# Optimization experiments

Measured on AMD Instinct MI355X. Metric: run time of the kernel, lower is better.

Reference implementation:

```python
import jax, jax.numpy as jnp
import numpy as np

N_NODES = 50000
N_EDGES = 800000
IN_CH = 512
HIDDEN = 512


def setup_inputs() -> dict:
    key = jax.random.key(0)
    k1, k2, k3, k4 = jax.random.split(key, 4)
    x = jax.random.normal(k1, (N_NODES, IN_CH), dtype=jnp.float32)
    edge_index = jax.random.randint(k2, (2, N_EDGES), 0, N_NODES, dtype=jnp.int64)
    # Glorot-style scaling for weights
    W1 = jax.random.normal(k3, (IN_CH, HIDDEN), dtype=jnp.float32) / np.sqrt(IN_CH)
    b1 = jnp.zeros((HIDDEN,), dtype=jnp.float32)
    W2 = jax.random.normal(k4, (HIDDEN, 1), dtype=jnp.float32) / np.sqrt(HIDDEN)
    b2 = jnp.zeros((1,), dtype=jnp.float32)
    return {"x": x, "edge_index": edge_index, "W1": W1, "b1": b1, "W2": W2, "b2": b2}


def _gcn_conv(x, edge_index, W, b):
    """PyG GCNConv: add self-loops, symmetric D^{-1/2}(A+I)D^{-1/2} normalization."""
    N = x.shape[0]
    xw = x @ W                                   # [N, out]
    row, col = edge_index[0], edge_index[1]      # source -> target
    # degree on target nodes, +1 for the self-loop
    deg = jax.ops.segment_sum(jnp.ones_like(col, dtype=xw.dtype), col, num_segments=N) + 1.0
    dis = jax.lax.rsqrt(deg)                     # deg^{-1/2}, [N]
    norm = dis[row] * dis[col]                   # [E]
    agg = jax.ops.segment_sum(norm[:, None] * xw[row], col, num_segments=N)
    agg = agg + (dis * dis)[:, None] * xw        # self-loop contribution
    return agg + b


def reference(x, edge_index, W1, b1, W2, b2):
    h = jax.nn.relu(_gcn_conv(x, edge_index, W1, b1))
    # dropout in eval mode (training=False) -> identity
    out = _gcn_conv(h, edge_index, W2, b2)
    return out.squeeze(-1)                       # [N]
```

## Files before the change

kernel.cpp:

```cpp
#include <hip/hip_runtime.h>

#define IN_CH 512
#define SCAN_BLK 1024

typedef _Float16 f16x8 __attribute__((ext_vector_type(8)));
typedef float f32x4 __attribute__((ext_vector_type(4)));

__device__ __forceinline__ void gload_lds16(const void* g, void* l) {
    __builtin_amdgcn_global_load_lds(
        (const __attribute__((address_space(1))) unsigned int*)g,
        (__attribute__((address_space(3))) unsigned int*)l, 16, 0, 0);
}

__global__ void k_deg(const int* __restrict__ col, int* __restrict__ deg,
                      int E, int N) {
    int e = blockIdx.x * blockDim.x + threadIdx.x;
    if (e < E) {
        int d = col[e];
        if ((unsigned)d < (unsigned)N) atomicAdd(&deg[d], 1);
    }
}

__global__ __launch_bounds__(SCAN_BLK) void k_psum(const int* __restrict__ deg,
                                                   int* __restrict__ bsum, int N) {
    __shared__ int red[SCAN_BLK / 64];
    int i = blockIdx.x * SCAN_BLK + threadIdx.x;
    int v = (i < N) ? deg[i] : 0;
#pragma unroll
    for (int off = 32; off > 0; off >>= 1) v += __shfl_down(v, off);
    if ((threadIdx.x & 63) == 0) red[threadIdx.x >> 6] = v;
    __syncthreads();
    if (threadIdx.x == 0) {
        int s = 0;
#pragma unroll
        for (int u = 0; u < SCAN_BLK / 64; ++u) s += red[u];
        bsum[blockIdx.x] = s;
    }
}

__global__ __launch_bounds__(SCAN_BLK) void k_write(const int* __restrict__ deg,
                                                    const int* __restrict__ bsum,
                                                    int* __restrict__ rp,
                                                    float* __restrict__ dis,
                                                    int* __restrict__ cursor, int N) {
    __shared__ int sums[SCAN_BLK];
    __shared__ int boff_s, tot_s;
    int t = threadIdx.x;
    if (t < 64) {
        int v = (t < (int)gridDim.x) ? bsum[t] : 0;
        int pre = (t < (int)blockIdx.x) ? v : 0;
        int a = pre, b = v;
#pragma unroll
        for (int off = 32; off > 0; off >>= 1) {
            a += __shfl_down(a, off);
            b += __shfl_down(b, off);
        }
        if (t == 0) { boff_s = a; tot_s = b; }
    }
    int i = blockIdx.x * SCAN_BLK + t;
    int d = (i < N) ? deg[i] : 0;
    sums[t] = d;
    __syncthreads();
    for (int off = 1; off < SCAN_BLK; off <<= 1) {
        int u = (t >= off) ? sums[t - off] : 0;
        __syncthreads();
        sums[t] += u;
        __syncthreads();
    }
    if (i < N) {
        rp[i] = boff_s + sums[t] - d;
        dis[i] = rsqrtf((float)d + 1.0f);
        cursor[i] = 0;
    }
    if (blockIdx.x == gridDim.x - 1 && t == 0) rp[N] = tot_s;
}

__global__ void k_fill(const int* __restrict__ ei, const int* __restrict__ rp,
                       int* __restrict__ cursor, int* __restrict__ csrc,
                       int E, int N) {
    int e = blockIdx.x * blockDim.x + threadIdx.x;
    if (e < E) {
        int s = ei[e];
        int d = ei[E + e];
        if ((unsigned)s < (unsigned)N && (unsigned)d < (unsigned)N) {
            int pos = atomicAdd(&cursor[d], 1);
            csrc[rp[d] + pos] = s;
        }
    }
}

__global__ __launch_bounds__(256) void k_cvt_w(const float* __restrict__ W1,
                                               _Float16* __restrict__ W1t) {
    __shared__ float tile[32][33];
    const int bk = blockIdx.x * 32, bn = blockIdx.y * 32;
    const int tx = threadIdx.x & 31, ty = threadIdx.x >> 5;
#pragma unroll
    for (int p = 0; p < 4; ++p)
        tile[ty + p * 8][tx] = W1[(size_t)(bk + ty + p * 8) * 512 + bn + tx];
    __syncthreads();
#pragma unroll
    for (int p = 0; p < 4; ++p)
        W1t[(size_t)(bn + ty + p * 8) * 512 + bk + tx] = (_Float16)tile[tx][ty + p * 8];
}

__global__ __launch_bounds__(256) void k_gemm(const float* __restrict__ A,
                                              const _Float16* __restrict__ Bt,
                                              const float* __restrict__ dis,
                                              _Float16* __restrict__ C,
                                              int Nrows, int nbm) {
    __shared__ __align__(16) _Float16 As[128 * 64];
    __shared__ __align__(16) _Float16 Bs[128 * 64];
    const int t = threadIdx.x;
    const int lane = t & 63, w = t >> 6;
    const int wm = w >> 1, wn = w & 1;

    const int nwg = nbm * 4;
    const int q = nwg >> 3, r = nwg & 7;
    const int xcd = blockIdx.x & 7, within = blockIdx.x >> 3;
    const int wg = (xcd < r ? xcd * (q + 1) : r * (q + 1) + (xcd - r) * q) + within;
    const int bm = (wg >> 2) * 128, bn = (wg & 3) * 128;

    const int rr = lane & 15, kg = lane >> 4;
    const int lrow = lane >> 3, lcol = (lane & 7) * 8;
    const int arow = t >> 3, acol = (t & 7) * 8;

    f32x4 acc[4][4];
#pragma unroll
    for (int i = 0; i < 4; ++i)
#pragma unroll
        for (int j = 0; j < 4; ++j) acc[i][j] = (f32x4)0.0f;

    for (int k0 = 0; k0 < 512; k0 += 64) {
#pragma unroll
        for (int p = 0; p < 4; ++p) {
            const int row = p * 32 + w * 8 + lrow;
            gload_lds16(Bt + (size_t)(bn + row) * 512 + k0 + lcol,
                        Bs + (p * 32 + w * 8) * 64);
        }
#pragma unroll
        for (int p = 0; p < 4; ++p) {
            int grow = bm + p * 32 + arow;
            if (grow >= Nrows) grow = Nrows - 1;
            const float* gp = A + (size_t)grow * 512 + k0 + acol;
            float4 u0 = *(const float4*)gp;
            float4 u1 = *(const float4*)(gp + 4);
            f16x8 o;
            o[0] = (_Float16)u0.x; o[1] = (_Float16)u0.y;
            o[2] = (_Float16)u0.z; o[3] = (_Float16)u0.w;
            o[4] = (_Float16)u1.x; o[5] = (_Float16)u1.y;
            o[6] = (_Float16)u1.z; o[7] = (_Float16)u1.w;
            *(f16x8*)(As + ((p * 32 + arow) * 64 + acol)) = o;
        }
        __syncthreads();
#pragma unroll
        for (int kk = 0; kk < 2; ++kk) {
            f16x8 a[4], b[4];
#pragma unroll
            for (int i = 0; i < 4; ++i)
                a[i] = *(const f16x8*)(As + (wm * 64 + i * 16 + rr) * 64 + kk * 32 + kg * 8);
#pragma unroll
            for (int j = 0; j < 4; ++j)
                b[j] = *(const f16x8*)(Bs + (wn * 64 + j * 16 + rr) * 64 + kk * 32 + kg * 8);
#pragma unroll
            for (int i = 0; i < 4; ++i)
#pragma unroll
                for (int j = 0; j < 4; ++j)
                    acc[i][j] = __builtin_amdgcn_mfma_f32_16x16x32_f16(a[i], b[j], acc[i][j], 0, 0, 0);
        }
        __syncthreads();
    }

#pragma unroll
    for (int i = 0; i < 4; ++i)
#pragma unroll
        for (int reg = 0; reg < 4; ++reg) {
            int m = bm + wm * 64 + i * 16 + kg * 4 + reg;
            int mc = (m < Nrows) ? m : Nrows - 1;
            float dm = dis[mc];
#pragma unroll
            for (int j = 0; j < 4; ++j) {
                int n = bn + wn * 64 + j * 16 + rr;
                C[(size_t)m * 512 + n] = (_Float16)(acc[i][j][reg] * dm);
            }
        }
}

__global__ __launch_bounds__(256) void k_agg(const _Float16* __restrict__ y,
                                             const float* __restrict__ dis,
                                             const int* __restrict__ rp,
                                             const int* __restrict__ csrc,
                                             const float* __restrict__ b1,
                                             const float* __restrict__ W2,
                                             float* __restrict__ z, int N) {
    const int n = blockIdx.x * 4 + (threadIdx.x >> 6);
    if (n >= N) return;
    const int l = threadIdx.x & 63;

    const float d1 = dis[n];
    f16x8 self = *(const f16x8*)(y + (size_t)n * 512 + l * 8);
    float acc[8];
#pragma unroll
    for (int c = 0; c < 8; ++c) acc[c] = (float)self[c];

    int j = rp[n], jend = rp[n + 1];
    for (; j + 8 <= jend; j += 8) {
        int s[8]; f16x8 v[8];
#pragma unroll
        for (int u = 0; u < 8; ++u) s[u] = csrc[j + u];
#pragma unroll
        for (int u = 0; u < 8; ++u)
            v[u] = *(const f16x8*)(y + (size_t)s[u] * 512 + l * 8);
#pragma unroll
        for (int u = 0; u < 8; ++u)
#pragma unroll
            for (int c = 0; c < 8; ++c) acc[c] += (float)v[u][c];
    }
    for (; j + 2 <= jend; j += 2) {
        int s0 = csrc[j], s1 = csrc[j + 1];
        f16x8 v0 = *(const f16x8*)(y + (size_t)s0 * 512 + l * 8);
        f16x8 v1 = *(const f16x8*)(y + (size_t)s1 * 512 + l * 8);
#pragma unroll
        for (int c = 0; c < 8; ++c) acc[c] += (float)v0[c] + (float)v1[c];
    }
    if (j < jend) {
        f16x8 v0 = *(const f16x8*)(y + (size_t)csrc[j] * 512 + l * 8);
#pragma unroll
        for (int c = 0; c < 8; ++c) acc[c] += (float)v0[c];
    }

    float4 bb0 = *(const float4*)(b1 + l * 8);
    float4 bb1 = *(const float4*)(b1 + l * 8 + 4);
    float4 w20 = *(const float4*)(W2 + l * 8);
    float4 w21 = *(const float4*)(W2 + l * 8 + 4);
    float bbv[8] = {bb0.x, bb0.y, bb0.z, bb0.w, bb1.x, bb1.y, bb1.z, bb1.w};
    float w2v[8] = {w20.x, w20.y, w20.z, w20.w, w21.x, w21.y, w21.z, w21.w};
    float p = 0.0f;
#pragma unroll
    for (int c = 0; c < 8; ++c) {
        float h = fmaxf(acc[c] * d1 + bbv[c], 0.0f);
        p += h * w2v[c];
    }
#pragma unroll
    for (int off = 32; off > 0; off >>= 1) p += __shfl_down(p, off);
    if (l == 0) z[n] = d1 * p;
}

__global__ void k_out(const float* __restrict__ z, const float* __restrict__ dis,
                      const int* __restrict__ rp, const int* __restrict__ csrc,
                      const float* __restrict__ b2, float* __restrict__ out, int N) {
    int n = blockIdx.x * blockDim.x + threadIdx.x;
    if (n >= N) return;
    float acc = z[n];
    int j = rp[n], jend = rp[n + 1];
    for (; j + 4 <= jend; j += 4) {
        float a0 = z[csrc[j]];
        float a1 = z[csrc[j + 1]];
        float a2 = z[csrc[j + 2]];
        float a3 = z[csrc[j + 3]];
        acc += (a0 + a1) + (a2 + a3);
    }
    for (; j < jend; ++j) acc += z[csrc[j]];
    out[n] = dis[n] * acc + b2[0];
}

extern "C" void kernel_launch(void* const* d_in, const int* in_sizes, int n_in,
                              void* d_out, int out_size, void* d_ws, size_t ws_size,
                              hipStream_t stream) {
    const float* x  = (const float*)d_in[0];
    const int*   ei = (const int*)d_in[1];
    const float* W1 = (const float*)d_in[2];
    const float* b1 = (const float*)d_in[3];
    const float* W2 = (const float*)d_in[4];
    const float* b2 = (const float*)d_in[5];
    float* out = (float*)d_out;

    const int N = in_sizes[0] / IN_CH;
    const int E = in_sizes[1] / 2;
    const int nbm = (N + 127) / 128;
    const int M2 = nbm * 128;
    const int NB = (N + SCAN_BLK - 1) / SCAN_BLK;

    char* ws = (char*)d_ws;
    size_t off = 0;
    auto alloc = [&](size_t bytes) {
        char* p = ws + off;
        off += (bytes + 255) & ~(size_t)255;
        return p;
    };
    _Float16* y   = (_Float16*)alloc((size_t)M2 * 512 * sizeof(_Float16));
    _Float16* W1t = (_Float16*)alloc((size_t)512 * 512 * sizeof(_Float16));
    int*   deg    = (int*)alloc((size_t)N * sizeof(int));
    float* dis    = (float*)alloc((size_t)N * sizeof(float));
    int*   rp     = (int*)alloc((size_t)(N + 1) * sizeof(int));
    int*   cursor = (int*)alloc((size_t)N * sizeof(int));
    int*   csrc   = (int*)alloc((size_t)E * sizeof(int));
    float* z      = (float*)alloc((size_t)N * sizeof(float));
    int*   bsum   = (int*)alloc((size_t)64 * sizeof(int));

    hipMemsetAsync(deg, 0, (size_t)N * sizeof(int), stream);

    k_deg<<<(E + 255) / 256, 256, 0, stream>>>(ei + E, deg, E, N);
    k_psum<<<NB, SCAN_BLK, 0, stream>>>(deg, bsum, N);
    k_write<<<NB, SCAN_BLK, 0, stream>>>(deg, bsum, rp, dis, cursor, N);
    k_fill<<<(E + 255) / 256, 256, 0, stream>>>(ei, rp, cursor, csrc, E, N);
    k_cvt_w<<<dim3(16, 16), 256, 0, stream>>>(W1, W1t);
    k_gemm<<<nbm * 4, 256, 0, stream>>>(x, W1t, dis, y, N, nbm);
    k_agg<<<(N + 3) / 4, 256, 0, stream>>>(y, dis, rp, csrc, b1, W2, z, N);
    k_out<<<(N + 255) / 256, 256, 0, stream>>>(z, dis, rp, csrc, b2, out, N);
}
```

Before: 272.9 us.

## Merge degree counting into GEMM launch and move source normalization into aggregation

The degree-count atomics now run as extra blocks appended to the GEMM grid, so the GEMM no longer depends on dis and the two independent jobs share one launch. To make that possible, the per-row dis scaling is dropped from the GEMM epilogue, and the aggregation kernel instead loads dis[src] for every edge and weights each gathered row by it. This removes one launch and lets the atomic traffic overlap the GEMM, at the cost of an extra scattered scalar load and multiplies per edge in the aggregation.

```diff
diff --git a/kernel.cpp b/kernel.cpp
--- a/kernel.cpp
+++ b/kernel.cpp
@@ -10,15 +10,6 @@
     __builtin_amdgcn_global_load_lds(
         (const __attribute__((address_space(1))) unsigned int*)g,
         (__attribute__((address_space(3))) unsigned int*)l, 16, 0, 0);
-}
-
-__global__ void k_deg(const int* __restrict__ col, int* __restrict__ deg,
-                      int E, int N) {
-    int e = blockIdx.x * blockDim.x + threadIdx.x;
-    if (e < E) {
-        int d = col[e];
-        if ((unsigned)d < (unsigned)N) atomicAdd(&deg[d], 1);
-    }
 }
 
 __global__ __launch_bounds__(SCAN_BLK) void k_psum(const int* __restrict__ deg,
@@ -103,18 +94,29 @@
         W1t[(size_t)(bn + ty + p * 8) * 512 + bk + tx] = (_Float16)tile[tx][ty + p * 8];
 }
 
-__global__ __launch_bounds__(256) void k_gemm(const float* __restrict__ A,
-                                              const _Float16* __restrict__ Bt,
-                                              const float* __restrict__ dis,
-                                              _Float16* __restrict__ C,
-                                              int Nrows, int nbm) {
+__global__ __launch_bounds__(256) void k_merged(const float* __restrict__ A,
+                                                const _Float16* __restrict__ Bt,
+                                                _Float16* __restrict__ C,
+                                                int Nrows, int nbm,
+                                                const int* __restrict__ col,
+                                                int* __restrict__ deg, int E, int N) {
     __shared__ __align__(16) _Float16 As[128 * 64];
     __shared__ __align__(16) _Float16 Bs[128 * 64];
+    const int nwg = nbm * 4;
+
+    if ((int)blockIdx.x >= nwg) {
+        int e = ((int)blockIdx.x - nwg) * 256 + threadIdx.x;
+        if (e < E) {
+            int d = col[e];
+            if ((unsigned)d < (unsigned)N) atomicAdd(&deg[d], 1);
+        }
+        return;
+    }
+
     const int t = threadIdx.x;
     const int lane = t & 63, w = t >> 6;
     const int wm = w >> 1, wn = w & 1;
 
-    const int nwg = nbm * 4;
     const int q = nwg >> 3, r = nwg & 7;
     const int xcd = blockIdx.x & 7, within = blockIdx.x >> 3;
     const int wg = (xcd < r ? xcd * (q + 1) : r * (q + 1) + (xcd - r) * q) + within;
@@ -173,16 +175,13 @@
 #pragma unroll
     for (int i = 0; i < 4; ++i)
 #pragma unroll
-        for (int reg = 0; reg < 4; ++reg) {
-            int m = bm + wm * 64 + i * 16 + kg * 4 + reg;
-            int mc = (m < Nrows) ? m : Nrows - 1;
-            float dm = dis[mc];
-#pragma unroll
-            for (int j = 0; j < 4; ++j) {
+        for (int j = 0; j < 4; ++j)
+#pragma unroll
+            for (int reg = 0; reg < 4; ++reg) {
+                int m = bm + wm * 64 + i * 16 + kg * 4 + reg;
                 int n = bn + wn * 64 + j * 16 + rr;
-                C[(size_t)m * 512 + n] = (_Float16)(acc[i][j][reg] * dm);
+                C[(size_t)m * 512 + n] = (_Float16)acc[i][j][reg];
             }
-        }
 }
 
 __global__ __launch_bounds__(256) void k_agg(const _Float16* __restrict__ y,
@@ -200,32 +199,37 @@
     f16x8 self = *(const f16x8*)(y + (size_t)n * 512 + l * 8);
     float acc[8];
 #pragma unroll
-    for (int c = 0; c < 8; ++c) acc[c] = (float)self[c];
+    for (int c = 0; c < 8; ++c) acc[c] = d1 * (float)self[c];
 
     int j = rp[n], jend = rp[n + 1];
     for (; j + 8 <= jend; j += 8) {
-        int s[8]; f16x8 v[8];
+        int s[8]; float wt[8]; f16x8 v[8];
 #pragma unroll
         for (int u = 0; u < 8; ++u) s[u] = csrc[j + u];
+#pragma unroll
+        for (int u = 0; u < 8; ++u) wt[u] = dis[s[u]];
 #pragma unroll
         for (int u = 0; u < 8; ++u)
             v[u] = *(const f16x8*)(y + (size_t)s[u] * 512 + l * 8);
 #pragma unroll
         for (int u = 0; u < 8; ++u)
 #pragma unroll
-            for (int c = 0; c < 8; ++c) acc[c] += (float)v[u][c];
+            for (int c = 0; c < 8; ++c) acc[c] += wt[u] * (float)v[u][c];
     }
     for (; j + 2 <= jend; j += 2) {
         int s0 = csrc[j], s1 = csrc[j + 1];
+        float w0 = dis[s0], w1 = dis[s1];
         f16x8 v0 = *(const f16x8*)(y + (size_t)s0 * 512 + l * 8);
         f16x8 v1 = *(const f16x8*)(y + (size_t)s1 * 512 + l * 8);
 #pragma unroll
-        for (int c = 0; c < 8; ++c) acc[c] += (float)v0[c] + (float)v1[c];
+        for (int c = 0; c < 8; ++c) acc[c] += w0 * (float)v0[c] + w1 * (float)v1[c];
     }
     if (j < jend) {
-        f16x8 v0 = *(const f16x8*)(y + (size_t)csrc[j] * 512 + l * 8);
-#pragma unroll
-        for (int c = 0; c < 8; ++c) acc[c] += (float)v0[c];
+        int s0 = csrc[j];
+        float w0 = dis[s0];
+        f16x8 v0 = *(const f16x8*)(y + (size_t)s0 * 512 + l * 8);
+#pragma unroll
+        for (int c = 0; c < 8; ++c) acc[c] += w0 * (float)v0[c];
     }
 
     float4 bb0 = *(const float4*)(b1 + l * 8);
@@ -279,6 +283,7 @@
     const int nbm = (N + 127) / 128;
     const int M2 = nbm * 128;
     const int NB = (N + SCAN_BLK - 1) / SCAN_BLK;
+    const int DEGB = (E + 255) / 256;
 
     char* ws = (char*)d_ws;
     size_t off = 0;
@@ -299,12 +304,12 @@
 
     hipMemsetAsync(deg, 0, (size_t)N * sizeof(int), stream);
 
-    k_deg<<<(E + 255) / 256, 256, 0, stream>>>(ei + E, deg, E, N);
+    k_cvt_w<<<dim3(16, 16), 256, 0, stream>>>(W1, W1t);
+    k_merged<<<nbm * 4 + DEGB, 256, 0, stream>>>(x, W1t, y, N, nbm,
+                                                 ei + E, deg, E, N);
     k_psum<<<NB, SCAN_BLK, 0, stream>>>(deg, bsum, N);
     k_write<<<NB, SCAN_BLK, 0, stream>>>(deg, bsum, rp, dis, cursor, N);
     k_fill<<<(E + 255) / 256, 256, 0, stream>>>(ei, rp, cursor, csrc, E, N);
-    k_cvt_w<<<dim3(16, 16), 256, 0, stream>>>(W1, W1t);
-    k_gemm<<<nbm * 4, 256, 0, stream>>>(x, W1t, dis, y, N, nbm);
     k_agg<<<(N + 3) / 4, 256, 0, stream>>>(y, dis, rp, csrc, b1, W2, z, N);
     k_out<<<(N + 255) / 256, 256, 0, stream>>>(z, dis, rp, csrc, b2, out, N);
 }
```

Measured after the change: 265.5 us. -2.7%, faster.
